# Kernel tuning notes

Hardware: AMD Instinct MI355X
Metric: run time of the kernel (lower is better)

## Reference

```python
import jax, jax.numpy as jnp
import numpy as np

B, N, E = 4, 2048, 512
H = 8
HD = E // H  # 64
SCALE = HD ** -0.5


def setup_inputs() -> dict:
    key = jax.random.key(0)
    k1, k2, k3 = jax.random.split(key, 3)
    x = jax.random.normal(k1, (B, N, E), dtype=jnp.float32)
    # xavier-uniform-like scaling for weights
    w_qkv = jax.random.normal(k2, (3 * E, E), dtype=jnp.float32) * (2.0 / (4 * E)) ** 0.5
    b_qkv = jnp.zeros((3 * E,), dtype=jnp.float32)
    w_out = jax.random.normal(k3, (E, E), dtype=jnp.float32) * (1.0 / E) ** 0.5
    b_out = jnp.zeros((E,), dtype=jnp.float32)
    return {"x": x, "w_qkv": w_qkv, "b_qkv": b_qkv, "w_out": w_out, "b_out": b_out}


def reference(x, w_qkv, b_qkv, w_out, b_out):
    b_sz, n_patches, _ = x.shape
    # qkv projection: [B,N,3E] -> [B,N,3,H,HD] -> [B,H,3,N,HD]
    qkv = (jnp.einsum('bne,fe->bnf', x, w_qkv) + b_qkv)
    qkv = qkv.reshape(b_sz, n_patches, 3, H, HD).transpose(0, 3, 2, 1, 4)
    q, k, v = qkv[:, :, 0], qkv[:, :, 1], qkv[:, :, 2]  # each [B,H,N,HD]
    attn = jnp.einsum('bhqd,bhkd->bhqk', q * SCALE, k)  # [B,H,N,N]
    attn = jax.nn.softmax(attn, axis=-1)
    # attn_dropout p=0.0 -> identity in reference
    out = jnp.einsum('bhqk,bhkd->bhqd', attn, v)  # [B,H,N,HD]
    out = out.transpose(0, 2, 1, 3).reshape(b_sz, n_patches, E)
    out = jnp.einsum('bne,fe->bnf', out, w_out) + b_out
    return out
```

## Files before the change

### kernel.cpp

```cpp
#include <hip/hip_runtime.h>

#define BB   4
#define SEQ  2048
#define EMB  512
#define NH   8
#define HD   64
#define QSCALE 0.18033688011f

typedef __bf16 bf16x8 __attribute__((ext_vector_type(8)));
typedef float  f32x4  __attribute__((ext_vector_type(4)));

__device__ __forceinline__ short f2bf(float f) {
  union { float f; unsigned u; } v; v.f = f;
  unsigned r = v.u + 0x7fffu + ((v.u >> 16) & 1u);
  return (short)(r >> 16);
}

__device__ __forceinline__ unsigned pk_bf16(float a, float b) {
#if __has_builtin(__builtin_amdgcn_cvt_pk_bf16_f32)
  typedef __bf16 bf16v2 __attribute__((ext_vector_type(2)));
  union { bf16v2 v; unsigned u; } cv;
  cv.v = __builtin_amdgcn_cvt_pk_bf16_f32(a, b);
  return cv.u;
#else
  return (unsigned)(unsigned short)f2bf(a) | ((unsigned)(unsigned short)f2bf(b) << 16);
#endif
}

__device__ __forceinline__ float fexp2(float x) {
#if __has_builtin(__builtin_amdgcn_exp2f)
  return __builtin_amdgcn_exp2f(x);
#else
  return exp2f(x);
#endif
}

__device__ __forceinline__ void gl_lds16(const void* g, void* l) {
  __builtin_amdgcn_global_load_lds(
      (const __attribute__((address_space(1))) unsigned int*)g,
      (__attribute__((address_space(3))) unsigned int*)l, 16, 0, 0);
}

__device__ __forceinline__ void quad_redist(unsigned &a, unsigned &b) {
  asm volatile("v_permlane32_swap_b32 %0, %1" : "+v"(a), "+v"(b));
  asm volatile("v_permlane16_swap_b32 %0, %1" : "+v"(a), "+v"(b));
}

__global__ __launch_bounds__(256) void cast_all(const float* __restrict__ x,
                                                const float* __restrict__ wq,
                                                const float* __restrict__ wo,
                                                short* __restrict__ xb,
                                                short* __restrict__ wqb,
                                                short* __restrict__ wob) {
  int i = blockIdx.x * 256 + threadIdx.x;
  const float* src; short* dst; int off;
  if (i < 1048576)      { src = x;  dst = xb;  off = i; }
  else if (i < 1245184) { src = wq; dst = wqb; off = i - 1048576; }
  else                  { src = wo; dst = wob; off = i - 1245184; }
  float4 v = ((const float4*)src)[off];
  uint2 o; o.x = pk_bf16(v.x, v.y); o.y = pk_bf16(v.z, v.w);
  *(uint2*)&dst[off * 4] = o;
}

__global__ __launch_bounds__(256) void qkv_gemm(const short* __restrict__ A,
                                                const short* __restrict__ W,
                                                const float* __restrict__ bias,
                                                short* __restrict__ qo,
                                                short* __restrict__ ko,
                                                short* __restrict__ vto) {
  __shared__ __align__(16) short As[128 * 64];
  __shared__ __align__(16) short Bs[128 * 64];
  const int tid  = threadIdx.x;
  const int lane = tid & 63, wave = tid >> 6;
  const int wm = wave >> 1, wf = wave & 1;
  const int col = lane & 15, quad = lane >> 4;
  const int m0 = blockIdx.x * 128, f0 = blockIdx.y * 128;

  const short* aSrc[4]; const short* wSrc[4];
#pragma unroll
  for (int rd = 0; rd < 4; ++rd) {
    int slot = rd * 256 + tid;
    int row = slot >> 3;
    int cb  = (slot & 7) ^ (row & 7);
    aSrc[rd] = A + (size_t)(m0 + row) * 512 + cb * 8;
    wSrc[rd] = W + (size_t)(f0 + row) * 512 + cb * 8;
  }
  int aOff[2][4], bOff[2][4];
#pragma unroll
  for (int kk = 0; kk < 2; ++kk)
#pragma unroll
    for (int i = 0; i < 4; ++i) {
      aOff[kk][i] = (wm * 64 + i * 16 + col) * 64 + (((kk * 4 + quad) ^ (col & 7)) * 8);
      bOff[kk][i] = (wf * 64 + i * 16 + col) * 64 + (((kk * 4 + quad) ^ (col & 7)) * 8);
    }

  f32x4 acc[4][4];
#pragma unroll
  for (int i = 0; i < 4; ++i)
#pragma unroll
    for (int j = 0; j < 4; ++j)
#pragma unroll
      for (int r = 0; r < 4; ++r) acc[i][j][r] = 0.f;

  for (int kt = 0; kt < 8; ++kt) {
    __syncthreads();
#pragma unroll
    for (int rd = 0; rd < 4; ++rd) {
      gl_lds16(aSrc[rd], (char*)As + rd * 4096 + wave * 1024);
      gl_lds16(wSrc[rd], (char*)Bs + rd * 4096 + wave * 1024);
      aSrc[rd] += 64; wSrc[rd] += 64;
    }
    __syncthreads();
#pragma unroll
    for (int kk = 0; kk < 2; ++kk) {
      bf16x8 af[4], bw[4];
#pragma unroll
      for (int i = 0; i < 4; ++i) af[i] = *(const bf16x8*)&As[aOff[kk][i]];
#pragma unroll
      for (int j = 0; j < 4; ++j) bw[j] = *(const bf16x8*)&Bs[bOff[kk][j]];
#pragma unroll
      for (int i = 0; i < 4; ++i)
#pragma unroll
        for (int j = 0; j < 4; ++j)
          acc[i][j] = __builtin_amdgcn_mfma_f32_16x16x32_bf16(af[i], bw[j], acc[i][j], 0, 0, 0);
    }
  }

#pragma unroll
  for (int j = 0; j < 4; ++j) {
    const int f = f0 + wf * 64 + j * 16 + col;
    const float bv = bias[f];
    const int sIdx = f >> 9;
    const int h = (f >> 6) & 7;
    const int d = f & 63;
#pragma unroll
    for (int i = 0; i < 4; ++i) {
      const int mbase = m0 + wm * 64 + i * 16 + quad * 4;
      const int b = mbase >> 11;
      const int n = mbase & 2047;
      const size_t bh = (size_t)(b * NH + h);
      if (sIdx == 2) {
        uint2 pk;
        pk.x = pk_bf16(acc[i][j][0] + bv, acc[i][j][1] + bv);
        pk.y = pk_bf16(acc[i][j][2] + bv, acc[i][j][3] + bv);
        *(uint2*)&vto[(bh * HD + d) * SEQ + n] = pk;
      } else if (sIdx == 0) {
#pragma unroll
        for (int r = 0; r < 4; ++r)
          qo[(bh * SEQ + n + r) * HD + d] = f2bf((acc[i][j][r] + bv) * QSCALE);
      } else {
#pragma unroll
        for (int r = 0; r < 4; ++r)
          ko[(bh * SEQ + n + r) * HD + d] = f2bf(acc[i][j][r] + bv);
      }
    }
  }
}

__global__ __launch_bounds__(512) void attn_kernel(const short* __restrict__ q,
                                                   const short* __restrict__ k,
                                                   const short* __restrict__ vt,
                                                   short* __restrict__ o) {
  __shared__ __align__(16) short Ks0[64 * 64];
  __shared__ __align__(16) short Vs0[64 * 64];
  __shared__ __align__(16) short Ks1[64 * 64];
  __shared__ __align__(16) short Vs1[64 * 64];

  const int tid  = threadIdx.x;
  const int lane = tid & 63, wave = tid >> 6;
  const int col = lane & 15, quad = lane >> 4;
  const int bh = blockIdx.x & 31;
  const int q0 = (blockIdx.x >> 5) * 128;
  const size_t bhBase = (size_t)bh * SEQ * HD;

  bf16x8 qf[2];
#pragma unroll
  for (int ks = 0; ks < 2; ++ks)
    qf[ks] = *(const bf16x8*)&q[bhBase +
        (size_t)(q0 + wave * 16 + col) * HD + ks * 32 + quad * 8];

  const int row = tid >> 3, cb = (tid & 7) ^ (row & 7);
  const short* ksrc = k  + bhBase + (size_t)row * HD  + cb * 8;
  const short* vsrc = vt + bhBase + (size_t)row * SEQ + cb * 8;
  char* const ldsK0 = (char*)Ks0 + wave * 1024;
  char* const ldsV0 = (char*)Vs0 + wave * 1024;
  char* const ldsK1 = (char*)Ks1 + wave * 1024;
  char* const ldsV1 = (char*)Vs1 + wave * 1024;

  f32x4 oacc[4];
#pragma unroll
  for (int nt = 0; nt < 4; ++nt)
#pragma unroll
    for (int r = 0; r < 4; ++r) oacc[nt][r] = 0.f;
  float lsum = 0.f;

  auto compute = [&](const short* KB, const short* VB) {
    f32x4 sacc[4];
#pragma unroll
    for (int kt = 0; kt < 4; ++kt)
#pragma unroll
      for (int r = 0; r < 4; ++r) sacc[kt][r] = 0.f;
#pragma unroll
    for (int ks = 0; ks < 2; ++ks)
#pragma unroll
      for (int kt = 0; kt < 4; ++kt) {
        bf16x8 kf = *(const bf16x8*)&KB[(kt * 16 + col) * 64 +
                                        (((ks * 4 + quad) ^ (col & 7)) * 8)];
        sacc[kt] = __builtin_amdgcn_mfma_f32_16x16x32_bf16(kf, qf[ks], sacc[kt], 0, 0, 0);
      }

    unsigned u[4][2];
#pragma unroll
    for (int kt = 0; kt < 4; ++kt) {
      float p0 = fexp2(sacc[kt][0]);
      float p1 = fexp2(sacc[kt][1]);
      float p2 = fexp2(sacc[kt][2]);
      float p3 = fexp2(sacc[kt][3]);
      lsum += (p0 + p1) + (p2 + p3);
      u[kt][0] = pk_bf16(p0, p1);
      u[kt][1] = pk_bf16(p2, p3);
    }

    union { unsigned w[4]; bf16x8 v; } pf0, pf1;
    {
      unsigned a, b;
      a = u[0][0]; b = u[1][0]; quad_redist(a, b); pf0.w[0] = a; pf0.w[2] = b;
      a = u[0][1]; b = u[1][1]; quad_redist(a, b); pf0.w[1] = a; pf0.w[3] = b;
      a = u[2][0]; b = u[3][0]; quad_redist(a, b); pf1.w[0] = a; pf1.w[2] = b;
      a = u[2][1]; b = u[3][1]; quad_redist(a, b); pf1.w[1] = a; pf1.w[3] = b;
    }

#pragma unroll
    for (int nt = 0; nt < 4; ++nt) {
      bf16x8 vf0 = *(const bf16x8*)&VB[(nt * 16 + col) * 64 +
                                       ((quad ^ (col & 7)) * 8)];
      oacc[nt] = __builtin_amdgcn_mfma_f32_16x16x32_bf16(pf0.v, vf0, oacc[nt], 0, 0, 0);
      bf16x8 vf1 = *(const bf16x8*)&VB[(nt * 16 + col) * 64 +
                                       (((4 + quad) ^ (col & 7)) * 8)];
      oacc[nt] = __builtin_amdgcn_mfma_f32_16x16x32_bf16(pf1.v, vf1, oacc[nt], 0, 0, 0);
    }
  };

  gl_lds16(ksrc, ldsK0); gl_lds16(vsrc, ldsV0);
  ksrc += 64 * HD; vsrc += 64;
  __syncthreads();

  for (int t = 0; t < 32; t += 2) {
    gl_lds16(ksrc, ldsK1); gl_lds16(vsrc, ldsV1);
    ksrc += 64 * HD; vsrc += 64;
    compute(Ks0, Vs0);
    __syncthreads();
    gl_lds16(ksrc, ldsK0); gl_lds16(vsrc, ldsV0);
    ksrc += 64 * HD; vsrc += 64;
    compute(Ks1, Vs1);
    __syncthreads();
  }

  lsum += __shfl_xor(lsum, 16);
  lsum += __shfl_xor(lsum, 32);

  const int b = bh >> 3, h = bh & 7;
#pragma unroll
  for (int r = 0; r < 4; ++r) {
    const float rl = 1.0f / __shfl(lsum, quad * 4 + r);
    const int n = q0 + wave * 16 + quad * 4 + r;
#pragma unroll
    for (int nt = 0; nt < 4; ++nt)
      o[((size_t)(b * SEQ + n)) * EMB + h * HD + nt * 16 + col] = f2bf(oacc[nt][r] * rl);
  }
}

__global__ __launch_bounds__(256) void proj_gemm(const short* __restrict__ A,
                                                 const short* __restrict__ W,
                                                 const float* __restrict__ bias,
                                                 float* __restrict__ out) {
  __shared__ __align__(16) short As[64 * 64];
  __shared__ __align__(16) short Bs[128 * 64];
  const int tid  = threadIdx.x;
  const int lane = tid & 63, wave = tid >> 6;
  const int wm = wave >> 1, wf = wave & 1;
  const int col = lane & 15, quad = lane >> 4;
  const int m0 = blockIdx.x * 64, f0 = blockIdx.y * 128;

  const short* aSrc[2]; const short* wSrc[4];
#pragma unroll
  for (int rd = 0; rd < 2; ++rd) {
    int slot = rd * 256 + tid;
    int row = slot >> 3;
    int cb  = (slot & 7) ^ (row & 7);
    aSrc[rd] = A + (size_t)(m0 + row) * 512 + cb * 8;
  }
#pragma unroll
  for (int rd = 0; rd < 4; ++rd) {
    int slot = rd * 256 + tid;
    int row = slot >> 3;
    int cb  = (slot & 7) ^ (row & 7);
    wSrc[rd] = W + (size_t)(f0 + row) * 512 + cb * 8;
  }
  int aOff[2][2], bOff[2][4];
#pragma unroll
  for (int kk = 0; kk < 2; ++kk) {
#pragma unroll
    for (int i = 0; i < 2; ++i)
      aOff[kk][i] = (wm * 32 + i * 16 + col) * 64 + (((kk * 4 + quad) ^ (col & 7)) * 8);
#pragma unroll
    for (int j = 0; j < 4; ++j)
      bOff[kk][j] = (wf * 64 + j * 16 + col) * 64 + (((kk * 4 + quad) ^ (col & 7)) * 8);
  }

  f32x4 acc[2][4];
#pragma unroll
  for (int i = 0; i < 2; ++i)
#pragma unroll
    for (int j = 0; j < 4; ++j)
#pragma unroll
      for (int r = 0; r < 4; ++r) acc[i][j][r] = 0.f;

  for (int kt = 0; kt < 8; ++kt) {
    __syncthreads();
#pragma unroll
    for (int rd = 0; rd < 2; ++rd) {
      gl_lds16(aSrc[rd], (char*)As + rd * 4096 + wave * 1024);
      aSrc[rd] += 64;
    }
#pragma unroll
    for (int rd = 0; rd < 4; ++rd) {
      gl_lds16(wSrc[rd], (char*)Bs + rd * 4096 + wave * 1024);
      wSrc[rd] += 64;
    }
    __syncthreads();
#pragma unroll
    for (int kk = 0; kk < 2; ++kk) {
      bf16x8 af[2], bw[4];
#pragma unroll
      for (int i = 0; i < 2; ++i) af[i] = *(const bf16x8*)&As[aOff[kk][i]];
#pragma unroll
      for (int j = 0; j < 4; ++j) bw[j] = *(const bf16x8*)&Bs[bOff[kk][j]];
#pragma unroll
      for (int i = 0; i < 2; ++i)
#pragma unroll
        for (int j = 0; j < 4; ++j)
          acc[i][j] = __builtin_amdgcn_mfma_f32_16x16x32_bf16(af[i], bw[j], acc[i][j], 0, 0, 0);
    }
  }

#pragma unroll
  for (int j = 0; j < 4; ++j) {
    const int f = f0 + wf * 64 + j * 16 + col;
    const float bv = bias[f];
#pragma unroll
    for (int i = 0; i < 2; ++i) {
      const int mbase = m0 + wm * 32 + i * 16 + quad * 4;
#pragma unroll
      for (int r = 0; r < 4; ++r)
        out[(size_t)(mbase + r) * 512 + f] = acc[i][j][r] + bv;
    }
  }
}

extern "C" void kernel_launch(void* const* d_in, const int* in_sizes, int n_in,
                              void* d_out, int out_size, void* d_ws, size_t ws_size,
                              hipStream_t stream) {
  (void)in_sizes; (void)n_in; (void)out_size; (void)ws_size;
  const float* x     = (const float*)d_in[0];
  const float* w_qkv = (const float*)d_in[1];
  const float* b_qkv = (const float*)d_in[2];
  const float* w_out = (const float*)d_in[3];
  const float* b_out = (const float*)d_in[4];
  float* out = (float*)d_out;

  char* ws = (char*)d_ws;
  short* xb    = (short*)(ws + 0);
  short* wqkvb = (short*)(ws + 8388608);
  short* woutb = (short*)(ws + 9961472);
  short* qb    = (short*)(ws + 10485760);
  short* kb    = (short*)(ws + 18874368);
  short* vtb   = (short*)(ws + 27262976);
  short* ob    = (short*)(ws + 35651584);

  cast_all<<<5120, 256, 0, stream>>>(x, w_qkv, w_out, xb, wqkvb, woutb);
  qkv_gemm<<<dim3(64, 12), 256, 0, stream>>>(xb, wqkvb, b_qkv, qb, kb, vtb);
  attn_kernel<<<512, 512, 0, stream>>>(qb, kb, vtb, ob);
  proj_gemm<<<dim3(128, 4), 256, 0, stream>>>(ob, woutb, b_out, out);
}
```

Baseline: 161.9 us.

## Double-buffer LDS tiles in QKV and output projection GEMMs

Both projection GEMMs now split the K loop into 32-wide stages and alternate between two LDS buffers. The next stage's global-to-LDS load is issued before computing on the current buffer, which removes one barrier per step and overlaps memory latency with MFMA work. The swizzle is changed to suit 32-element rows. The last iteration issues a redundant wraparound load of stage 0, and the smaller stages mean more barriers per K element.

```diff
diff --git a/kernel.cpp b/kernel.cpp
--- a/kernel.cpp
+++ b/kernel.cpp
@@ -68,31 +68,32 @@
                                                 short* __restrict__ qo,
                                                 short* __restrict__ ko,
                                                 short* __restrict__ vto) {
-  __shared__ __align__(16) short As[128 * 64];
-  __shared__ __align__(16) short Bs[128 * 64];
+  __shared__ __align__(16) short As0[128 * 32];
+  __shared__ __align__(16) short Bs0[128 * 32];
+  __shared__ __align__(16) short As1[128 * 32];
+  __shared__ __align__(16) short Bs1[128 * 32];
   const int tid  = threadIdx.x;
   const int lane = tid & 63, wave = tid >> 6;
   const int wm = wave >> 1, wf = wave & 1;
   const int col = lane & 15, quad = lane >> 4;
   const int m0 = blockIdx.x * 128, f0 = blockIdx.y * 128;
 
-  const short* aSrc[4]; const short* wSrc[4];
-#pragma unroll
-  for (int rd = 0; rd < 4; ++rd) {
+  const short* aSrc[2]; const short* wSrc[2];
+#pragma unroll
+  for (int rd = 0; rd < 2; ++rd) {
     int slot = rd * 256 + tid;
-    int row = slot >> 3;
-    int cb  = (slot & 7) ^ (row & 7);
+    int row  = slot >> 2;
+    int cb   = (slot & 3) ^ ((slot >> 3) & 3);
     aSrc[rd] = A + (size_t)(m0 + row) * 512 + cb * 8;
     wSrc[rd] = W + (size_t)(f0 + row) * 512 + cb * 8;
   }
-  int aOff[2][4], bOff[2][4];
-#pragma unroll
-  for (int kk = 0; kk < 2; ++kk)
-#pragma unroll
-    for (int i = 0; i < 4; ++i) {
-      aOff[kk][i] = (wm * 64 + i * 16 + col) * 64 + (((kk * 4 + quad) ^ (col & 7)) * 8);
-      bOff[kk][i] = (wf * 64 + i * 16 + col) * 64 + (((kk * 4 + quad) ^ (col & 7)) * 8);
-    }
+  int aOff[4], bOff[4];
+  const int rc = (quad ^ ((col >> 1) & 3)) * 8;
+#pragma unroll
+  for (int i = 0; i < 4; ++i) {
+    aOff[i] = (wm * 64 + i * 16 + col) * 32 + rc;
+    bOff[i] = (wf * 64 + i * 16 + col) * 32 + rc;
+  }
 
   f32x4 acc[4][4];
 #pragma unroll
@@ -102,29 +103,39 @@
 #pragma unroll
       for (int r = 0; r < 4; ++r) acc[i][j][r] = 0.f;
 
-  for (int kt = 0; kt < 8; ++kt) {
-    __syncthreads();
-#pragma unroll
-    for (int rd = 0; rd < 4; ++rd) {
-      gl_lds16(aSrc[rd], (char*)As + rd * 4096 + wave * 1024);
-      gl_lds16(wSrc[rd], (char*)Bs + rd * 4096 + wave * 1024);
-      aSrc[rd] += 64; wSrc[rd] += 64;
-    }
-    __syncthreads();
-#pragma unroll
-    for (int kk = 0; kk < 2; ++kk) {
-      bf16x8 af[4], bw[4];
-#pragma unroll
-      for (int i = 0; i < 4; ++i) af[i] = *(const bf16x8*)&As[aOff[kk][i]];
-#pragma unroll
-      for (int j = 0; j < 4; ++j) bw[j] = *(const bf16x8*)&Bs[bOff[kk][j]];
-#pragma unroll
-      for (int i = 0; i < 4; ++i)
-#pragma unroll
-        for (int j = 0; j < 4; ++j)
-          acc[i][j] = __builtin_amdgcn_mfma_f32_16x16x32_bf16(af[i], bw[j], acc[i][j], 0, 0, 0);
-    }
-  }
+#define QSTAGE(BUFA, BUFB, KS)                                         \
+  {                                                                    \
+    const int ko_ = (KS) * 32;                                         \
+    gl_lds16(aSrc[0] + ko_, (char*)(BUFA) + wave * 1024);              \
+    gl_lds16(aSrc[1] + ko_, (char*)(BUFA) + 4096 + wave * 1024);       \
+    gl_lds16(wSrc[0] + ko_, (char*)(BUFB) + wave * 1024);              \
+    gl_lds16(wSrc[1] + ko_, (char*)(BUFB) + 4096 + wave * 1024);       \
+  }
+
+  auto qcompute = [&](const short* As, const short* Bs) {
+    bf16x8 af[4], bw[4];
+#pragma unroll
+    for (int i = 0; i < 4; ++i) af[i] = *(const bf16x8*)&As[aOff[i]];
+#pragma unroll
+    for (int j = 0; j < 4; ++j) bw[j] = *(const bf16x8*)&Bs[bOff[j]];
+#pragma unroll
+    for (int i = 0; i < 4; ++i)
+#pragma unroll
+      for (int j = 0; j < 4; ++j)
+        acc[i][j] = __builtin_amdgcn_mfma_f32_16x16x32_bf16(af[i], bw[j], acc[i][j], 0, 0, 0);
+  };
+
+  QSTAGE(As0, Bs0, 0);
+  __syncthreads();
+  for (int t = 0; t < 16; t += 2) {
+    QSTAGE(As1, Bs1, t + 1);
+    qcompute(As0, Bs0);
+    __syncthreads();
+    QSTAGE(As0, Bs0, (t + 2) & 15);
+    qcompute(As1, Bs1);
+    __syncthreads();
+  }
+#undef QSTAGE
 
 #pragma unroll
   for (int j = 0; j < 4; ++j) {
@@ -274,75 +285,79 @@
                                                  const short* __restrict__ W,
                                                  const float* __restrict__ bias,
                                                  float* __restrict__ out) {
-  __shared__ __align__(16) short As[64 * 64];
-  __shared__ __align__(16) short Bs[128 * 64];
+  __shared__ __align__(16) short As0[64 * 32];
+  __shared__ __align__(16) short Bs0[128 * 32];
+  __shared__ __align__(16) short As1[64 * 32];
+  __shared__ __align__(16) short Bs1[128 * 32];
   const int tid  = threadIdx.x;
   const int lane = tid & 63, wave = tid >> 6;
   const int wm = wave >> 1, wf = wave & 1;
   const int col = lane & 15, quad = lane >> 4;
   const int m0 = blockIdx.x * 64, f0 = blockIdx.y * 128;
 
-  const short* aSrc[2]; const short* wSrc[4];
+  const short* aSrcP;
+  {
+    int row = tid >> 2;
+    int cb  = (tid & 3) ^ ((tid >> 3) & 3);
+    aSrcP = A + (size_t)(m0 + row) * 512 + cb * 8;
+  }
+  const short* wSrcP[2];
 #pragma unroll
   for (int rd = 0; rd < 2; ++rd) {
     int slot = rd * 256 + tid;
-    int row = slot >> 3;
-    int cb  = (slot & 7) ^ (row & 7);
-    aSrc[rd] = A + (size_t)(m0 + row) * 512 + cb * 8;
-  }
-#pragma unroll
-  for (int rd = 0; rd < 4; ++rd) {
-    int slot = rd * 256 + tid;
-    int row = slot >> 3;
-    int cb  = (slot & 7) ^ (row & 7);
-    wSrc[rd] = W + (size_t)(f0 + row) * 512 + cb * 8;
-  }
-  int aOff[2][2], bOff[2][4];
-#pragma unroll
-  for (int kk = 0; kk < 2; ++kk) {
+    int row  = slot >> 2;
+    int cb   = (slot & 3) ^ ((slot >> 3) & 3);
+    wSrcP[rd] = W + (size_t)(f0 + row) * 512 + cb * 8;
+  }
+  int aOff[2], bOff[4];
+  const int rc = (quad ^ ((col >> 1) & 3)) * 8;
+#pragma unroll
+  for (int i = 0; i < 2; ++i)
+    aOff[i] = (wm * 32 + i * 16 + col) * 32 + rc;
+#pragma unroll
+  for (int j = 0; j < 4; ++j)
+    bOff[j] = (wf * 64 + j * 16 + col) * 32 + rc;
+
+  f32x4 acc[2][4];
+#pragma unroll
+  for (int i = 0; i < 2; ++i)
+#pragma unroll
+    for (int j = 0; j < 4; ++j)
+#pragma unroll
+      for (int r = 0; r < 4; ++r) acc[i][j][r] = 0.f;
+
+#define PSTAGE(BUFA, BUFB, KS)                                         \
+  {                                                                    \
+    const int ko_ = (KS) * 32;                                         \
+    gl_lds16(aSrcP + ko_, (char*)(BUFA) + wave * 1024);                \
+    gl_lds16(wSrcP[0] + ko_, (char*)(BUFB) + wave * 1024);             \
+    gl_lds16(wSrcP[1] + ko_, (char*)(BUFB) + 4096 + wave * 1024);      \
+  }
+
+  auto pcompute = [&](const short* As, const short* Bs) {
+    bf16x8 af[2], bw[4];
+#pragma unroll
+    for (int i = 0; i < 2; ++i) af[i] = *(const bf16x8*)&As[aOff[i]];
+#pragma unroll
+    for (int j = 0; j < 4; ++j) bw[j] = *(const bf16x8*)&Bs[bOff[j]];
 #pragma unroll
     for (int i = 0; i < 2; ++i)
-      aOff[kk][i] = (wm * 32 + i * 16 + col) * 64 + (((kk * 4 + quad) ^ (col & 7)) * 8);
-#pragma unroll
-    for (int j = 0; j < 4; ++j)
-      bOff[kk][j] = (wf * 64 + j * 16 + col) * 64 + (((kk * 4 + quad) ^ (col & 7)) * 8);
-  }
-
-  f32x4 acc[2][4];
-#pragma unroll
-  for (int i = 0; i < 2; ++i)
-#pragma unroll
-    for (int j = 0; j < 4; ++j)
-#pragma unroll
-      for (int r = 0; r < 4; ++r) acc[i][j][r] = 0.f;
-
-  for (int kt = 0; kt < 8; ++kt) {
-    __syncthreads();
-#pragma unroll
-    for (int rd = 0; rd < 2; ++rd) {
-      gl_lds16(aSrc[rd], (char*)As + rd * 4096 + wave * 1024);
-      aSrc[rd] += 64;
-    }
-#pragma unroll
-    for (int rd = 0; rd < 4; ++rd) {
-      gl_lds16(wSrc[rd], (char*)Bs + rd * 4096 + wave * 1024);
-      wSrc[rd] += 64;
-    }
-    __syncthreads();
-#pragma unroll
-    for (int kk = 0; kk < 2; ++kk) {
-      bf16x8 af[2], bw[4];
-#pragma unroll
-      for (int i = 0; i < 2; ++i) af[i] = *(const bf16x8*)&As[aOff[kk][i]];
-#pragma unroll
-      for (int j = 0; j < 4; ++j) bw[j] = *(const bf16x8*)&Bs[bOff[kk][j]];
-#pragma unroll
-      for (int i = 0; i < 2; ++i)
-#pragma unroll
-        for (int j = 0; j < 4; ++j)
-          acc[i][j] = __builtin_amdgcn_mfma_f32_16x16x32_bf16(af[i], bw[j], acc[i][j], 0, 0, 0);
-    }
-  }
+#pragma unroll
+      for (int j = 0; j < 4; ++j)
+        acc[i][j] = __builtin_amdgcn_mfma_f32_16x16x32_bf16(af[i], bw[j], acc[i][j], 0, 0, 0);
+  };
+
+  PSTAGE(As0, Bs0, 0);
+  __syncthreads();
+  for (int t = 0; t < 16; t += 2) {
+    PSTAGE(As1, Bs1, t + 1);
+    pcompute(As0, Bs0);
+    __syncthreads();
+    PSTAGE(As0, Bs0, (t + 2) & 15);
+    pcompute(As1, Bs1);
+    __syncthreads();
+  }
+#undef PSTAGE
 
 #pragma unroll
   for (int j = 0; j < 4; ++j) {
```

Measured after the change: 162.7 us. About the same (+0.5%).
